# Performance work log

Hardware: AMD Instinct MI355X
Metric: run time of the kernel (lower is better)

The kernel has to match this reference:

```python
import jax, jax.numpy as jnp
import numpy as np
from jax import lax

K = 3  # kernel_size
PAD = 1
STRIDE = 1
DIL = 1


def setup_inputs() -> dict:
    key = jax.random.key(0)
    k1, k2 = jax.random.split(key)
    x = jax.random.normal(k1, (32, 256, 56, 56), dtype=jnp.float32)
    weights = jax.random.normal(k2, (256, 256, K * K), dtype=jnp.float32) * 0.05
    return {"x": x, "weights": weights}


def reference(x, weights):
    B, C, H, W = x.shape
    O = weights.shape[0]
    # weights stored as [O, C, k*k] -> standard OIHW conv kernel
    w = weights.reshape(O, C, K, K)
    # Dense conv replaces the per-(channel, filter) matmul loop over im2col windows.
    y = lax.conv_general_dilated(
        x, w,
        window_strides=(STRIDE, STRIDE),
        padding=[(PAD, PAD), (PAD, PAD)],
        rhs_dilation=(DIL, DIL),
        dimension_numbers=("NCHW", "OIHW", "NCHW"),
    )  # [B, O, Hout, Wout]
    Hout, Wout = y.shape[2], y.shape[3]
    # Faithful to original: results buffer is laid out [O, B, Hout, Wout]
    # (out-channel-major blocks of batch) then reinterpreted as [B, O, Hout, Wout].
    result = jnp.transpose(y, (1, 0, 2, 3)).reshape(B, O, Hout, Wout)
    return result
```

## Files before the change

kernel.cpp:

```cpp
#include <hip/hip_runtime.h>
#include <hip/hip_bf16.h>

using s8v   = __attribute__((ext_vector_type(8))) short;
using f32x4 = __attribute__((ext_vector_type(4))) float;

#define N_TOT 100352
#define WT_ELEMS 589824
#define PLANE_ELEMS 861184
#define XT_ELEMS 27557888
#define WS_NEED  56295424

__device__ __forceinline__ unsigned short f2bf(float f) {
    unsigned int u = __float_as_uint(f);
    unsigned int r = (u + 0x7FFF + ((u >> 16) & 1)) >> 16;
    return (unsigned short)r;
}

__device__ __forceinline__ void gl_lds16(const void* g, void* l) {
    __builtin_amdgcn_global_load_lds(
        (const __attribute__((address_space(1))) unsigned int*)g,
        (__attribute__((address_space(3))) unsigned int*)l, 16, 0, 0);
}

__global__ void prep_w(const float* __restrict__ w, unsigned short* __restrict__ wt) {
    int idx = blockIdx.x * 256 + threadIdx.x;
    int sub   = idx & 7;
    int row   = (idx >> 3) & 127;
    int chunk = (idx >> 10) & 3;
    int kb    = (idx >> 12) % 72;
    int mt    = idx / 294912;
    int tap = kb >> 3, cb = kb & 7;
    int c = cb * 32 + chunk * 8 + sub;
    int o = mt * 128 + row;
    wt[idx] = f2bf(w[(o * 256 + c) * 9 + tap]);
}

__global__ void prep_x(const float* __restrict__ x, unsigned short* __restrict__ xt) {
    int b  = blockIdx.x / 58;
    int hp = blockIdx.x % 58;
    int tid = threadIdx.x;
    uint4 zero = {0u, 0u, 0u, 0u};
    size_t rowbase = (size_t)(b * 58 + hp) * 58;
    if (hp == 0 || hp == 57) {
        for (int i = tid; i < 1856; i += 256) {
            int cg = i / 58, wp = i - cg * 58;
            *(uint4*)(xt + ((size_t)cg * PLANE_ELEMS + (rowbase + wp) * 8)) = zero;
        }
        return;
    }
    int h = hp - 1;
    __shared__ unsigned short lds[56 * 264];
    #pragma unroll
    for (int it = 0; it < 14; ++it) {
        int idx = it * 256 + tid;
        int c  = idx / 14;
        int w4 = idx - c * 14;
        float4 v = *(const float4*)(x + (((size_t)(b * 256 + c) * 56 + h) * 56 + w4 * 4));
        int wb = w4 * 4;
        lds[(wb + 0) * 264 + c] = f2bf(v.x);
        lds[(wb + 1) * 264 + c] = f2bf(v.y);
        lds[(wb + 2) * 264 + c] = f2bf(v.z);
        lds[(wb + 3) * 264 + c] = f2bf(v.w);
    }
    __syncthreads();
    for (int i = tid; i < 1856; i += 256) {
        int cg = i / 58, wp = i - cg * 58;
        uint4 v;
        if (wp == 0 || wp == 57) v = zero;
        else v = *(const uint4*)&lds[(wp - 1) * 264 + cg * 8];
        *(uint4*)(xt + ((size_t)cg * PLANE_ELEMS + (rowbase + wp) * 8)) = v;
    }
}

__global__ __launch_bounds__(256) void gemm_conv(const unsigned short* __restrict__ wt,
                                                 const unsigned short* __restrict__ xt,
                                                 float* __restrict__ out) {
    __shared__ __align__(16) char smA[8192];
    __shared__ __align__(16) char smB[8192];
    int bx = blockIdx.x;
    int mt = bx / 784;
    int rb = bx - mt * 784;
    int nt = (rb & 7) * 98 + (rb >> 3);
    int tid  = threadIdx.x;
    int wave = tid >> 6, lane = tid & 63;
    int quad = lane >> 4, l16 = lane & 15;
    int wm = wave >> 1, wn = wave & 1;

    const unsigned short* aSrc = wt + (size_t)mt * 294912 + wave * 1024 + lane * 8;
    char* ldsA0 = smA + wave * 2048;
    char* ldsB0 = smB + wave * 2048;

    int n1 = nt * 128 + lane;
    int b1 = n1 / 3136; int r1 = n1 - b1 * 3136; int h1 = r1 / 56; int w1 = r1 - h1 * 56;
    int n2 = n1 + 64;
    int b2 = n2 / 3136; int r2 = n2 - b2 * 3136; int h2 = r2 / 56; int w2 = r2 - h2 * 56;
    size_t pix1 = (size_t)((b1 * 58 + h1) * 58 + w1) * 8;
    size_t pix2 = (size_t)((b2 * 58 + h2) * 58 + w2) * 8;

    const char* ra = smA + quad * 2048;
    const char* rb2 = smB + quad * 2048;

    f32x4 acc[4][4] = {};

    for (int tap = 0; tap < 9; ++tap) {
        int dh = tap / 3;
        int dw = tap - dh * 3;
        size_t tshift = (size_t)(dh * 58 + dw) * 8;
        for (int cb = 0; cb < 8; ++cb) {
            const unsigned short* plane = xt + (size_t)(cb * 4 + wave) * PLANE_ELEMS + tshift;
            gl_lds16(aSrc,        ldsA0);
            gl_lds16(aSrc + 512,  ldsA0 + 1024);
            gl_lds16(plane + pix1, ldsB0);
            gl_lds16(plane + pix2, ldsB0 + 1024);
            aSrc += 4096;
            __syncthreads();
            s8v af[4], bf[4];
            #pragma unroll
            for (int i = 0; i < 4; ++i)
                af[i] = *(const s8v*)(ra + ((wm * 64 + i * 16 + l16) << 4));
            #pragma unroll
            for (int j = 0; j < 4; ++j)
                bf[j] = *(const s8v*)(rb2 + ((wn * 64 + j * 16 + l16) << 4));
            #pragma unroll
            for (int i = 0; i < 4; ++i)
                #pragma unroll
                for (int j = 0; j < 4; ++j)
                    acc[i][j] = __builtin_amdgcn_mfma_f32_16x16x32_bf16(af[i], bf[j], acc[i][j], 0, 0, 0);
            __syncthreads();
        }
    }

    float* op = out + (size_t)(mt * 128 + wm * 64 + quad * 4) * N_TOT + nt * 128 + wn * 64 + l16;
    #pragma unroll
    for (int i = 0; i < 4; ++i)
        #pragma unroll
        for (int r = 0; r < 4; ++r) {
            float* orow = op + (size_t)(i * 16 + r) * N_TOT;
            #pragma unroll
            for (int j = 0; j < 4; ++j)
                orow[j * 16] = acc[i][j][r];
        }
}

__global__ void conv_naive(const float* __restrict__ x, const float* __restrict__ wq,
                           float* __restrict__ out) {
    int f = blockIdx.x * 256 + threadIdx.x;
    int o = f / N_TOT;
    int n = f - o * N_TOT;
    int b = n / 3136; int r = n - b * 3136; int h = r / 56; int w = r - h * 56;
    const float* xb = x + (size_t)b * 256 * 3136;
    const float* wo = wq + o * 2304;
    float acc = 0.f;
    for (int c = 0; c < 256; ++c) {
        const float* xc = xb + c * 3136;
        const float* wc = wo + c * 9;
        #pragma unroll
        for (int dh = 0; dh < 3; ++dh) {
            int ih = h + dh - 1;
            if (ih < 0 || ih >= 56) continue;
            const float* xr = xc + ih * 56;
            #pragma unroll
            for (int dw = 0; dw < 3; ++dw) {
                int iw = w + dw - 1;
                if (iw >= 0 && iw < 56) acc += xr[iw] * wc[dh * 3 + dw];
            }
        }
    }
    out[f] = acc;
}

extern "C" void kernel_launch(void* const* d_in, const int* in_sizes, int n_in,
                              void* d_out, int out_size, void* d_ws, size_t ws_size,
                              hipStream_t stream) {
    const float* x = (const float*)d_in[0];
    const float* w = (const float*)d_in[1];
    float* out = (float*)d_out;
    if (ws_size >= (size_t)WS_NEED) {
        unsigned short* wt = (unsigned short*)d_ws;
        unsigned short* xt = wt + WT_ELEMS;
        prep_w<<<2304, 256, 0, stream>>>(w, wt);
        prep_x<<<32 * 58, 256, 0, stream>>>(x, xt);
        gemm_conv<<<1568, 256, 0, stream>>>(wt, xt, out);
    } else {
        conv_naive<<<N_TOT, 256, 0, stream>>>(x, w, out);
    }
}
```

Measured before the change: 371.3 us.

## Reorder conv GEMM loop to channel-block outer, taps inner; simplify input repack

```diff
diff --git a/kernel.cpp b/kernel.cpp
--- a/kernel.cpp
+++ b/kernel.cpp
@@ -29,7 +29,7 @@
     int chunk = (idx >> 10) & 3;
     int kb    = (idx >> 12) % 72;
     int mt    = idx / 294912;
-    int tap = kb >> 3, cb = kb & 7;
+    int cb = kb / 9, tap = kb - cb * 9;
     int c = cb * 32 + chunk * 8 + sub;
     int o = mt * 128 + row;
     wt[idx] = f2bf(w[(o * 256 + c) * 9 + tap]);
@@ -49,26 +49,24 @@
         return;
     }
     int h = hp - 1;
-    __shared__ unsigned short lds[56 * 264];
-    #pragma unroll
-    for (int it = 0; it < 14; ++it) {
-        int idx = it * 256 + tid;
-        int c  = idx / 14;
-        int w4 = idx - c * 14;
-        float4 v = *(const float4*)(x + (((size_t)(b * 256 + c) * 56 + h) * 56 + w4 * 4));
-        int wb = w4 * 4;
-        lds[(wb + 0) * 264 + c] = f2bf(v.x);
-        lds[(wb + 1) * 264 + c] = f2bf(v.y);
-        lds[(wb + 2) * 264 + c] = f2bf(v.z);
-        lds[(wb + 3) * 264 + c] = f2bf(v.w);
-    }
-    __syncthreads();
-    for (int i = tid; i < 1856; i += 256) {
-        int cg = i / 58, wp = i - cg * 58;
-        uint4 v;
-        if (wp == 0 || wp == 57) v = zero;
-        else v = *(const uint4*)&lds[(wp - 1) * 264 + cg * 8];
-        *(uint4*)(xt + ((size_t)cg * PLANE_ELEMS + (rowbase + wp) * 8)) = v;
+    int wave = tid >> 6, lane = tid & 63;
+    for (int cg = wave; cg < 32; cg += 4) {
+        unsigned short* outp = xt + (size_t)cg * PLANE_ELEMS + rowbase * 8;
+        if (lane < 56) {
+            const float* src = x + ((size_t)(b * 256 + cg * 8) * 3136 + h * 56 + lane);
+            unsigned int p[4];
+            #pragma unroll
+            for (int q = 0; q < 4; ++q) {
+                float f0 = src[(size_t)(2 * q) * 3136];
+                float f1 = src[(size_t)(2 * q + 1) * 3136];
+                p[q] = (unsigned)f2bf(f0) | ((unsigned)f2bf(f1) << 16);
+            }
+            *(uint4*)(outp + (size_t)(lane + 1) * 8) = *(uint4*)p;
+        } else if (lane == 56) {
+            *(uint4*)outp = zero;
+        } else if (lane == 57) {
+            *(uint4*)(outp + 57 * 8) = zero;
+        }
     }
 }
 
@@ -97,36 +95,40 @@
     size_t pix1 = (size_t)((b1 * 58 + h1) * 58 + w1) * 8;
     size_t pix2 = (size_t)((b2 * 58 + h2) * 58 + w2) * 8;
 
-    const char* ra = smA + quad * 2048;
+    const char* ra  = smA + quad * 2048;
     const char* rb2 = smB + quad * 2048;
 
     f32x4 acc[4][4] = {};
 
-    for (int tap = 0; tap < 9; ++tap) {
-        int dh = tap / 3;
-        int dw = tap - dh * 3;
-        size_t tshift = (size_t)(dh * 58 + dw) * 8;
-        for (int cb = 0; cb < 8; ++cb) {
-            const unsigned short* plane = xt + (size_t)(cb * 4 + wave) * PLANE_ELEMS + tshift;
-            gl_lds16(aSrc,        ldsA0);
-            gl_lds16(aSrc + 512,  ldsA0 + 1024);
-            gl_lds16(plane + pix1, ldsB0);
-            gl_lds16(plane + pix2, ldsB0 + 1024);
-            aSrc += 4096;
-            __syncthreads();
-            s8v af[4], bf[4];
+    #pragma unroll 1
+    for (int cb = 0; cb < 8; ++cb) {
+        const unsigned short* pl1 = xt + (size_t)(cb * 4 + wave) * PLANE_ELEMS + pix1;
+        const unsigned short* pl2 = xt + (size_t)(cb * 4 + wave) * PLANE_ELEMS + pix2;
+        #pragma unroll
+        for (int dh = 0; dh < 3; ++dh) {
             #pragma unroll
-            for (int i = 0; i < 4; ++i)
-                af[i] = *(const s8v*)(ra + ((wm * 64 + i * 16 + l16) << 4));
-            #pragma unroll
-            for (int j = 0; j < 4; ++j)
-                bf[j] = *(const s8v*)(rb2 + ((wn * 64 + j * 16 + l16) << 4));
-            #pragma unroll
-            for (int i = 0; i < 4; ++i)
+            for (int dw = 0; dw < 3; ++dw) {
+                int tsh = (dh * 58 + dw) * 8;
+                gl_lds16(aSrc,        ldsA0);
+                gl_lds16(aSrc + 512,  ldsA0 + 1024);
+                gl_lds16(pl1 + tsh,   ldsB0);
+                gl_lds16(pl2 + tsh,   ldsB0 + 1024);
+                aSrc += 4096;
+                __syncthreads();
+                s8v af[4], bf[4];
+                #pragma unroll
+                for (int i = 0; i < 4; ++i)
+                    af[i] = *(const s8v*)(ra + ((wm * 64 + i * 16 + l16) << 4));
                 #pragma unroll
                 for (int j = 0; j < 4; ++j)
-                    acc[i][j] = __builtin_amdgcn_mfma_f32_16x16x32_bf16(af[i], bf[j], acc[i][j], 0, 0, 0);
-            __syncthreads();
+                    bf[j] = *(const s8v*)(rb2 + ((wn * 64 + j * 16 + l16) << 4));
+                #pragma unroll
+                for (int i = 0; i < 4; ++i)
+                    #pragma unroll
+                    for (int j = 0; j < 4; ++j)
+                        acc[i][j] = __builtin_amdgcn_mfma_f32_16x16x32_bf16(af[i], bf[j], acc[i][j], 0, 0, 0);
+                __syncthreads();
+            }
         }
     }
 
```

New measurement: 361.8 us. -2.6%, faster.
